# Performance work log

Hardware: AMD Instinct MI355X
Metric: run time of the kernel (lower is better)

## Reference

```python
import jax, jax.numpy as jnp
import numpy as np

N = 50000
E = 300000
HOPS = 3
LAYERS = 2
HEADS = 8
D_IN = 256
D_HID = 256
D_OUT = 256
D_HEAD = D_HID // HEADS
DECAY = [float(np.exp(-0.5 * k)) for k in range(HOPS)]  # hop_decay alpha = 0.5
LRELU_ACT = 0.01   # nn.LeakyReLU default slope (activation)
LRELU_ATT = 0.2    # GATConv attention leaky_relu slope
LN_EPS = 1e-5


def setup_inputs() -> dict:
    key = jax.random.key(0)
    ks = jax.random.split(key, 12)
    def sc(fan):
        return 1.0 / np.sqrt(fan)
    inp = {
        "x": jax.random.normal(ks[0], (N, D_IN), jnp.float32),
        "edge_index_k_hops": jax.random.randint(ks[1], (HOPS, 2, E), 0, N, jnp.int32),
        "lin1_w": jax.random.normal(ks[2], (D_IN, D_HID), jnp.float32) * sc(D_IN),
        "lin1_b": jnp.zeros((D_HID,), jnp.float32),
        "gat_w": jax.random.normal(ks[3], (LAYERS, HOPS, D_HID, D_HID), jnp.float32) * sc(D_HID),
        "gat_att_src": jax.random.normal(ks[4], (LAYERS, HOPS, HEADS, D_HEAD), jnp.float32) * sc(D_HEAD),
        "gat_att_dst": jax.random.normal(ks[5], (LAYERS, HOPS, HEADS, D_HEAD), jnp.float32) * sc(D_HEAD),
        "gat_bias": jnp.zeros((LAYERS, HOPS, D_HID), jnp.float32),
        "dec_w": jax.random.normal(ks[6], (LAYERS, HOPS, D_HID, D_OUT), jnp.float32) * sc(D_HID),
        "dec_b": jnp.zeros((LAYERS, HOPS, D_OUT), jnp.float32),
        "ln_scale": jnp.ones((LAYERS, D_OUT), jnp.float32),
        "ln_bias": jnp.zeros((LAYERS, D_OUT), jnp.float32),
    }
    return inp


def gat_conv(x, src, dst, W, a_src, a_dst, bias):
    # x: [N, D_HID]; src/dst: [E] ints. PyG GATConv (concat=True), eval mode.
    h = (x @ W).reshape(N, HEADS, D_HEAD)                  # [N, H, Dh]
    alpha_s = jnp.einsum('nhd,hd->nh', h, a_src)           # [N, H]
    alpha_d = jnp.einsum('nhd,hd->nh', h, a_dst)           # [N, H]
    e = jax.nn.leaky_relu(alpha_s[src] + alpha_d[dst], LRELU_ATT)  # [E, H]
    m = jax.ops.segment_max(e, dst, num_segments=N)        # segment softmax over dst
    e = jnp.exp(e - m[dst])
    s = jax.ops.segment_sum(e, dst, num_segments=N)
    a = e / (s[dst] + 1e-16)                               # [E, H]
    msg = h[src] * a[:, :, None]                           # [E, H, Dh]
    out = jax.ops.segment_sum(msg, dst, num_segments=N)    # [N, H, Dh]
    return out.reshape(N, D_HID) + bias


def layer_norm(x, scale, bias):
    mu = jnp.mean(x, axis=-1, keepdims=True)
    var = jnp.mean(jnp.square(x - mu), axis=-1, keepdims=True)
    return (x - mu) * jax.lax.rsqrt(var + LN_EPS) * scale + bias


def reference(x, edge_index_k_hops, lin1_w, lin1_b, gat_w, gat_att_src, gat_att_dst,
              gat_bias, dec_w, dec_b, ln_scale, ln_bias):
    h = jax.nn.leaky_relu(x @ lin1_w + lin1_b, LRELU_ACT)
    residual = h
    for l in range(LAYERS):
        acc = jnp.zeros((N, D_OUT), h.dtype)
        for k in range(HOPS):
            src = edge_index_k_hops[k, 0]
            dst = edge_index_k_hops[k, 1]
            xk = gat_conv(h, src, dst, gat_w[l, k], gat_att_src[l, k],
                          gat_att_dst[l, k], gat_bias[l, k])
            xk = jax.nn.leaky_relu(xk @ dec_w[l, k] + dec_b[l, k], LRELU_ACT)
            acc = acc + DECAY[k] * xk
        h = layer_norm(acc, ln_scale[l], ln_bias[l]) + residual
        residual = h
    return h
```

## Files before the change

### kernel.cpp

```cpp
#include <hip/hip_runtime.h>
#include <hip/hip_bf16.h>

#define NNODE 50000
#define NEDGE 300000
#define KPAD 40

static const float DECAY0 = 1.0f;
static const float DECAY1 = 0.60653065971263342f;
static const float DECAY2 = 0.36787944117144233f;

typedef __attribute__((ext_vector_type(8))) short bf16x8;
typedef __attribute__((ext_vector_type(4))) float f32x4;
typedef __attribute__((ext_vector_type(4))) unsigned short u16x4;

__device__ __forceinline__ unsigned split2(float f) {
    const unsigned u = __float_as_uint(f);
    const unsigned hi = u >> 16;
    const float fh = __uint_as_float(hi << 16);
    const unsigned lo = __float_as_uint(f - fh) >> 16;
    return (hi << 16) | lo;
}
__device__ __forceinline__ float bf2f(unsigned short u) {
    return __uint_as_float((unsigned)u << 16);
}

__global__ __launch_bounds__(256) void transpose_split_w(
    const float* __restrict__ gat_w, const float* __restrict__ dec_w,
    const float* __restrict__ lin1_w, unsigned short* __restrict__ Wp)
{
    const int m = blockIdx.z;
    const float* src = (m < 6) ? gat_w + (size_t)m * 65536
                     : (m < 12) ? dec_w + (size_t)(m - 6) * 65536
                                : lin1_w;
    unsigned short* dst = Wp + (size_t)m * 131072;
    __shared__ float tile[32][33];
    const int bx = blockIdx.x * 32;
    const int by = blockIdx.y * 32;
    const int tx = threadIdx.x & 31;
    const int ty = threadIdx.x >> 5;
#pragma unroll
    for (int i = 0; i < 32; i += 8)
        tile[ty + i][tx] = src[(size_t)(by + ty + i) * 256 + bx + tx];
    __syncthreads();
#pragma unroll
    for (int i = 0; i < 32; i += 8) {
        const int n = bx + ty + i, k = by + tx;
        const unsigned p = split2(tile[tx][ty + i]);
        dst[(size_t)n * 512 + k] = (unsigned short)(p >> 16);
        dst[(size_t)n * 512 + 256 + k] = (unsigned short)(p & 0xffffu);
    }
}

__global__ __launch_bounds__(256) void convert_split(
    const float* __restrict__ src, unsigned short* __restrict__ dst)
{
    const int gid = blockIdx.x * 256 + threadIdx.x;
    if (gid >= NNODE * 32) return;
    const int row = gid >> 5;
    const int k = (gid & 31) * 8;
    const float4 f0 = *reinterpret_cast<const float4*>(src + (size_t)row * 256 + k);
    const float4 f1 = *reinterpret_cast<const float4*>(src + (size_t)row * 256 + k + 4);
    u16x4 h0, h1, l0, l1;
    unsigned p;
    p = split2(f0.x); h0[0] = (unsigned short)(p >> 16); l0[0] = (unsigned short)p;
    p = split2(f0.y); h0[1] = (unsigned short)(p >> 16); l0[1] = (unsigned short)p;
    p = split2(f0.z); h0[2] = (unsigned short)(p >> 16); l0[2] = (unsigned short)p;
    p = split2(f0.w); h0[3] = (unsigned short)(p >> 16); l0[3] = (unsigned short)p;
    p = split2(f1.x); h1[0] = (unsigned short)(p >> 16); l1[0] = (unsigned short)p;
    p = split2(f1.y); h1[1] = (unsigned short)(p >> 16); l1[1] = (unsigned short)p;
    p = split2(f1.z); h1[2] = (unsigned short)(p >> 16); l1[2] = (unsigned short)p;
    p = split2(f1.w); h1[3] = (unsigned short)(p >> 16); l1[3] = (unsigned short)p;
    unsigned short* dh = dst + (size_t)row * 512 + k;
    *(u16x4*)dh = h0; *(u16x4*)(dh + 4) = h1;
    *(u16x4*)(dh + 256) = l0; *(u16x4*)(dh + 260) = l1;
}

__global__ __launch_bounds__(256) void gemm_pack(
    const unsigned short* __restrict__ Ap, const unsigned short* __restrict__ Wp,
    float* __restrict__ C, unsigned short* __restrict__ Cpack,
    int M, const float* __restrict__ out_bias,
    float slope, int do_act, int accum, float decay)
{
    __shared__ unsigned short Ah[128][KPAD];
    __shared__ unsigned short Al[128][KPAD];
    __shared__ unsigned short Bh[128][KPAD];
    __shared__ unsigned short Bl[128][KPAD];

    const int tid  = threadIdx.x;
    const int bm   = blockIdx.x * 128;
    const int bn   = blockIdx.y * 128;
    const int lane = tid & 63;
    const int w    = tid >> 6;
    const int wm   = w >> 1, wn = w & 1;
    const int srow = tid >> 1;
    const int skb  = (tid & 1) << 4;

    const bool aval = (bm + srow) < M;
    const unsigned short* ap = Ap + (size_t)(bm + srow) * 512 + skb;
    const unsigned short* bp = Wp + (size_t)(bn + srow) * 512 + skb;

    bf16x8 rAh0 = {0,0,0,0,0,0,0,0}, rAh1 = rAh0, rAl0 = rAh0, rAl1 = rAh0;
    bf16x8 rBh0, rBh1, rBl0, rBl1;

#define LOADT(K0)                                                        \
    do {                                                                 \
        if (aval) {                                                      \
            rAh0 = *(const bf16x8*)(ap + (K0));                          \
            rAh1 = *(const bf16x8*)(ap + (K0) + 8);                      \
            rAl0 = *(const bf16x8*)(ap + 256 + (K0));                    \
            rAl1 = *(const bf16x8*)(ap + 256 + (K0) + 8);                \
        }                                                                \
        rBh0 = *(const bf16x8*)(bp + (K0));                              \
        rBh1 = *(const bf16x8*)(bp + (K0) + 8);                          \
        rBl0 = *(const bf16x8*)(bp + 256 + (K0));                        \
        rBl1 = *(const bf16x8*)(bp + 256 + (K0) + 8);                    \
    } while (0)

    f32x4 acc[4][4];
#pragma unroll
    for (int mi = 0; mi < 4; mi++)
#pragma unroll
        for (int ni = 0; ni < 4; ni++) {
            acc[mi][ni][0] = 0.f; acc[mi][ni][1] = 0.f;
            acc[mi][ni][2] = 0.f; acc[mi][ni][3] = 0.f;
        }

    const int lrow = lane & 15;
    const int koff = (lane >> 4) << 3;

    LOADT(0);

    for (int kt = 0; kt < 8; kt++) {
        __syncthreads();
        *(bf16x8*)&Ah[srow][skb]     = rAh0;
        *(bf16x8*)&Ah[srow][skb + 8] = rAh1;
        *(bf16x8*)&Al[srow][skb]     = rAl0;
        *(bf16x8*)&Al[srow][skb + 8] = rAl1;
        *(bf16x8*)&Bh[srow][skb]     = rBh0;
        *(bf16x8*)&Bh[srow][skb + 8] = rBh1;
        *(bf16x8*)&Bl[srow][skb]     = rBl0;
        *(bf16x8*)&Bl[srow][skb + 8] = rBl1;
        __syncthreads();
        if (kt < 7) LOADT((kt + 1) * 32);

        bf16x8 fah[4], fal[4];
#pragma unroll
        for (int mi = 0; mi < 4; mi++) {
            const int r = 64 * wm + 16 * mi + lrow;
            fah[mi] = *(const bf16x8*)&Ah[r][koff];
            fal[mi] = *(const bf16x8*)&Al[r][koff];
        }
#pragma unroll
        for (int ni = 0; ni < 4; ni++) {
            const int r = 64 * wn + 16 * ni + lrow;
            const bf16x8 fbh = *(const bf16x8*)&Bh[r][koff];
            const bf16x8 fbl = *(const bf16x8*)&Bl[r][koff];
#pragma unroll
            for (int mi = 0; mi < 4; mi++) {
                acc[mi][ni] = __builtin_amdgcn_mfma_f32_16x16x32_bf16(fah[mi], fbh, acc[mi][ni], 0, 0, 0);
                acc[mi][ni] = __builtin_amdgcn_mfma_f32_16x16x32_bf16(fal[mi], fbh, acc[mi][ni], 0, 0, 0);
                acc[mi][ni] = __builtin_amdgcn_mfma_f32_16x16x32_bf16(fah[mi], fbl, acc[mi][ni], 0, 0, 0);
            }
        }
    }
#undef LOADT

    const int rb = bm + 64 * wm + ((lane >> 4) << 2);
    const int cb = bn + 64 * wn + (lane & 15);
#pragma unroll
    for (int ni = 0; ni < 4; ni++) {
        const int col = cb + 16 * ni;
        const float ob = out_bias ? out_bias[col] : 0.f;
#pragma unroll
        for (int mi = 0; mi < 4; mi++) {
#pragma unroll
            for (int r = 0; r < 4; r++) {
                const int row = rb + 16 * mi + r;
                if (row < M) {
                    float vv = acc[mi][ni][r] + ob;
                    if (do_act) vv = (vv > 0.f) ? vv : slope * vv;
                    vv *= decay;
                    if (Cpack) {
                        const unsigned p = split2(vv);
                        Cpack[(size_t)row * 512 + col] = (unsigned short)(p >> 16);
                        Cpack[(size_t)row * 512 + 256 + col] = (unsigned short)(p & 0xffffu);
                    } else if (accum) {
                        C[(size_t)row * 256 + col] += vv;
                    } else {
                        C[(size_t)row * 256 + col] = vv;
                    }
                }
            }
        }
    }
}

__global__ __launch_bounds__(256) void alpha_kernel(
    const float* __restrict__ hproj, const float* __restrict__ att_s,
    const float* __restrict__ att_d, float* __restrict__ alpha_s, float* __restrict__ alpha_d)
{
    const int n = blockIdx.x;
    const int t = threadIdx.x;
    const float v  = hproj[(size_t)n * 256 + t];
    float ps = v * att_s[t];
    float pd = v * att_d[t];
#pragma unroll
    for (int off = 16; off > 0; off >>= 1) {
        ps += __shfl_xor(ps, off, 32);
        pd += __shfl_xor(pd, off, 32);
    }
    if ((t & 31) == 0) {
        alpha_s[n * 8 + (t >> 5)] = ps;
        alpha_d[n * 8 + (t >> 5)] = pd;
    }
}

__global__ __launch_bounds__(256) void hist_kernel(
    const int* __restrict__ edges, int* __restrict__ hist)
{
    const int gid = blockIdx.x * 256 + threadIdx.x;
    if (gid >= 3 * NEDGE) return;
    const int k = gid / NEDGE;
    const int e = gid - k * NEDGE;
    const int d = edges[(size_t)k * 2 * NEDGE + NEDGE + e];
    atomicAdd(&hist[k * NNODE + d], 1);
}

__global__ __launch_bounds__(1024) void scan_kernel(
    const int* __restrict__ hist, int* __restrict__ row_ptr)
{
    const int hop = blockIdx.x;
    const int* hsrc = hist + hop * NNODE;
    int* rp = row_ptr + hop * (NNODE + 1);
    __shared__ int buf[1024];
    const int t = threadIdx.x;
    int offset = 0;
    for (int base = 0; base < NNODE; base += 1024) {
        const int idx = base + t;
        int v = (idx < NNODE) ? hsrc[idx] : 0;
        buf[t] = v;
        __syncthreads();
        for (int off = 1; off < 1024; off <<= 1) {
            int add = (t >= off) ? buf[t - off] : 0;
            __syncthreads();
            buf[t] += add;
            __syncthreads();
        }
        if (idx < NNODE) rp[idx] = offset + buf[t] - v;
        const int total = buf[1023];
        __syncthreads();
        offset += total;
    }
    if (t == 0) rp[NNODE] = offset;
}

__global__ __launch_bounds__(256) void cursor_kernel(
    const int* __restrict__ row_ptr, int* __restrict__ cursor)
{
    const int gid = blockIdx.x * 256 + threadIdx.x;
    if (gid >= 3 * NNODE) return;
    const int k = gid / NNODE;
    const int i = gid - k * NNODE;
    cursor[gid] = row_ptr[k * (NNODE + 1) + i];
}

__global__ __launch_bounds__(256) void fill_kernel(
    const int* __restrict__ edges, int* __restrict__ cursor, int* __restrict__ col)
{
    const int gid = blockIdx.x * 256 + threadIdx.x;
    if (gid >= 3 * NEDGE) return;
    const int k = gid / NEDGE;
    const int e = gid - k * NEDGE;
    const int s = edges[(size_t)k * 2 * NEDGE + e];
    const int d = edges[(size_t)k * 2 * NEDGE + NEDGE + e];
    const int pos = atomicAdd(&cursor[k * NNODE + d], 1);
    col[(size_t)k * NEDGE + pos] = s;
}

__global__ __launch_bounds__(256) void gat_gather(
    const int* __restrict__ row_ptr, const int* __restrict__ col,
    const float* __restrict__ alpha_s, const float* __restrict__ alpha_d,
    const float* __restrict__ hproj, const float* __restrict__ bias,
    unsigned short* __restrict__ outp)
{
    const int wave = (blockIdx.x * 256 + threadIdx.x) >> 6;
    const int lane = threadIdx.x & 63;
    if (wave >= NNODE) return;
    const int d = wave;
    const int h = lane >> 3;
    const float adh = alpha_d[d * 8 + h];
    const int beg = row_ptr[d];
    const int end = row_ptr[d + 1];

    float m = -3.402823466e38f;
    float s = 0.f;
    float a0 = 0.f, a1 = 0.f, a2 = 0.f, a3 = 0.f;

    for (int e = beg; e < end; ++e) {
        const int sidx = col[e];
        float v = alpha_s[sidx * 8 + h] + adh;
        v = (v > 0.f) ? v : 0.2f * v;
        if (v > m) {
            const float f = __expf(m - v);
            s *= f; a0 *= f; a1 *= f; a2 *= f; a3 *= f;
            m = v;
        }
        const float p = __expf(v - m);
        s += p;
        const float4 hv = *reinterpret_cast<const float4*>(hproj + (size_t)sidx * 256 + lane * 4);
        a0 += p * hv.x; a1 += p * hv.y; a2 += p * hv.z; a3 += p * hv.w;
    }
    const float inv = 1.f / (s + 1e-16f);
    const float b0 = bias[lane * 4 + 0], b1 = bias[lane * 4 + 1];
    const float b2 = bias[lane * 4 + 2], b3 = bias[lane * 4 + 3];
    u16x4 hi, lo;
    unsigned p0 = split2(a0 * inv + b0);
    unsigned p1 = split2(a1 * inv + b1);
    unsigned p2 = split2(a2 * inv + b2);
    unsigned p3 = split2(a3 * inv + b3);
    hi[0] = (unsigned short)(p0 >> 16); lo[0] = (unsigned short)p0;
    hi[1] = (unsigned short)(p1 >> 16); lo[1] = (unsigned short)p1;
    hi[2] = (unsigned short)(p2 >> 16); lo[2] = (unsigned short)p2;
    hi[3] = (unsigned short)(p3 >> 16); lo[3] = (unsigned short)p3;
    *(u16x4*)(outp + (size_t)d * 512 + lane * 4) = hi;
    *(u16x4*)(outp + (size_t)d * 512 + 256 + lane * 4) = lo;
}

__global__ __launch_bounds__(256) void ln_kernel(
    const float* __restrict__ accb, const unsigned short* __restrict__ hres,
    unsigned short* __restrict__ hout, float* __restrict__ final_out,
    const float* __restrict__ lns, const float* __restrict__ lnb)
{
    const int n = blockIdx.x;
    const int t = threadIdx.x;
    const float a = accb[(size_t)n * 256 + t];
    __shared__ float red[256];
    red[t] = a;
    __syncthreads();
    for (int off = 128; off > 0; off >>= 1) {
        if (t < off) red[t] += red[t + off];
        __syncthreads();
    }
    const float mu = red[0] * (1.f / 256.f);
    __syncthreads();
    const float dv = a - mu;
    red[t] = dv * dv;
    __syncthreads();
    for (int off = 128; off > 0; off >>= 1) {
        if (t < off) red[t] += red[t + off];
        __syncthreads();
    }
    const float var = red[0] * (1.f / 256.f);
    const float r = rsqrtf(var + 1e-5f);
    const float res = bf2f(hres[(size_t)n * 512 + t]) + bf2f(hres[(size_t)n * 512 + 256 + t]);
    const float o = dv * r * lns[t] + lnb[t] + res;
    if (final_out) {
        final_out[(size_t)n * 256 + t] = o;
    } else {
        const unsigned p = split2(o);
        hout[(size_t)n * 512 + t] = (unsigned short)(p >> 16);
        hout[(size_t)n * 512 + 256 + t] = (unsigned short)(p & 0xffffu);
    }
}

extern "C" void kernel_launch(void* const* d_in, const int* in_sizes, int n_in,
                              void* d_out, int out_size, void* d_ws, size_t ws_size,
                              hipStream_t stream) {
    const float* x      = (const float*)d_in[0];
    const int*   edges  = (const int*)  d_in[1];
    const float* lin1_w = (const float*)d_in[2];
    const float* lin1_b = (const float*)d_in[3];
    const float* gat_w  = (const float*)d_in[4];
    const float* att_s  = (const float*)d_in[5];
    const float* att_d  = (const float*)d_in[6];
    const float* gat_b  = (const float*)d_in[7];
    const float* dec_w  = (const float*)d_in[8];
    const float* dec_b  = (const float*)d_in[9];
    const float* ln_s   = (const float*)d_in[10];
    const float* ln_b   = (const float*)d_in[11];

    float* out = (float*)d_out;
    const size_t NF = (size_t)NNODE * 256;
    const size_t NP = (size_t)NNODE * 512;
    const size_t N8 = (size_t)NNODE * 8;

    float*          acc_buf = (float*)d_ws;
    float*          hproj   = acc_buf + NF;
    unsigned short* gpack   = (unsigned short*)(hproj + NF);
    unsigned short* hpack   = gpack + NP;
    unsigned short* wpack   = hpack + NP;
    float*          as_     = (float*)(wpack + (size_t)13 * 131072);
    float*          ad_     = as_ + N8;
    int*            hist    = (int*)(ad_ + N8);
    int*            cursor  = hist + 3 * NNODE;
    int*            row_ptr = cursor + 3 * NNODE;
    int*            col     = row_ptr + 3 * (NNODE + 1);

    const float decays[3] = {DECAY0, DECAY1, DECAY2};

    dim3 gg((NNODE + 127) / 128, 2);
    dim3 tg(8, 8, 13);
    const int e3b = (3 * NEDGE + 255) / 256;
    const int n3b = (3 * NNODE + 255) / 256;
    const int gb  = (NNODE * 64 + 255) / 256;
    const int cvb = (NNODE * 32 + 255) / 256;

    transpose_split_w<<<tg, 256, 0, stream>>>(gat_w, dec_w, lin1_w, wpack);
    convert_split<<<cvb, 256, 0, stream>>>(x, gpack);

    (void)hipMemsetAsync(hist, 0, 3 * NNODE * sizeof(int), stream);
    hist_kernel<<<e3b, 256, 0, stream>>>(edges, hist);
    scan_kernel<<<3, 1024, 0, stream>>>(hist, row_ptr);
    cursor_kernel<<<n3b, 256, 0, stream>>>(row_ptr, cursor);
    fill_kernel<<<e3b, 256, 0, stream>>>(edges, cursor, col);

    gemm_pack<<<gg, 256, 0, stream>>>(gpack, wpack + (size_t)12 * 131072, nullptr, hpack,
                                      NNODE, lin1_b, 0.01f, 1, 0, 1.f);

    for (int l = 0; l < 2; l++) {
        for (int k = 0; k < 3; k++) {
            const int lk = l * 3 + k;
            gemm_pack<<<gg, 256, 0, stream>>>(hpack, wpack + (size_t)lk * 131072, hproj, nullptr,
                                              NNODE, nullptr, 0.f, 0, 0, 1.f);
            alpha_kernel<<<NNODE, 256, 0, stream>>>(hproj, att_s + lk * 256, att_d + lk * 256,
                                                    as_, ad_);
            gat_gather<<<gb, 256, 0, stream>>>(row_ptr + (size_t)k * (NNODE + 1),
                                               col + (size_t)k * NEDGE,
                                               as_, ad_, hproj, gat_b + lk * 256, gpack);
            gemm_pack<<<gg, 256, 0, stream>>>(gpack, wpack + (size_t)(6 + lk) * 131072, acc_buf,
                                              nullptr, NNODE, dec_b + lk * 256,
                                              0.01f, 1, (k > 0) ? 1 : 0, decays[k]);
        }
        ln_kernel<<<NNODE, 256, 0, stream>>>(acc_buf, hpack, hpack,
                                             (l == 1) ? out : nullptr,
                                             ln_s + l * 256, ln_b + l * 256);
    }
}
```

Baseline: 1.686 ms.

## Store projected features as bf16 payload and parallelize CSR prefix scan

The GAT projection GEMM now writes round-to-nearest bf16 values instead of fp32, and the alpha and gather kernels read them. This halves the bytes moved in the edge-gather phase, which reads a random source row for every edge. The single-block sequential scan is replaced by a three-kernel block-local scan, block-sum scan and add that also fills the cursor array. The trade-off is lower precision in the aggregated features (bf16 instead of fp32) and a few extra kernel launches.

```diff
diff --git a/kernel.cpp b/kernel.cpp
--- a/kernel.cpp
+++ b/kernel.cpp
@@ -22,6 +22,10 @@
 }
 __device__ __forceinline__ float bf2f(unsigned short u) {
     return __uint_as_float((unsigned)u << 16);
+}
+__device__ __forceinline__ unsigned short rn_bf16(float f) {
+    const unsigned u = __float_as_uint(f);
+    return (unsigned short)((u + 0x7fffu + ((u >> 16) & 1u)) >> 16);
 }
 
 __global__ __launch_bounds__(256) void transpose_split_w(
@@ -78,6 +82,7 @@
 __global__ __launch_bounds__(256) void gemm_pack(
     const unsigned short* __restrict__ Ap, const unsigned short* __restrict__ Wp,
     float* __restrict__ C, unsigned short* __restrict__ Cpack,
+    unsigned short* __restrict__ payload,
     int M, const float* __restrict__ out_bias,
     float slope, int do_act, int accum, float decay)
 {
@@ -177,17 +182,21 @@
             for (int r = 0; r < 4; r++) {
                 const int row = rb + 16 * mi + r;
                 if (row < M) {
-                    float vv = acc[mi][ni][r] + ob;
-                    if (do_act) vv = (vv > 0.f) ? vv : slope * vv;
-                    vv *= decay;
-                    if (Cpack) {
-                        const unsigned p = split2(vv);
-                        Cpack[(size_t)row * 512 + col] = (unsigned short)(p >> 16);
-                        Cpack[(size_t)row * 512 + 256 + col] = (unsigned short)(p & 0xffffu);
-                    } else if (accum) {
-                        C[(size_t)row * 256 + col] += vv;
+                    if (payload) {
+                        payload[(size_t)row * 256 + col] = rn_bf16(acc[mi][ni][r]);
                     } else {
-                        C[(size_t)row * 256 + col] = vv;
+                        float vv = acc[mi][ni][r] + ob;
+                        if (do_act) vv = (vv > 0.f) ? vv : slope * vv;
+                        vv *= decay;
+                        if (Cpack) {
+                            const unsigned p = split2(vv);
+                            Cpack[(size_t)row * 512 + col] = (unsigned short)(p >> 16);
+                            Cpack[(size_t)row * 512 + 256 + col] = (unsigned short)(p & 0xffffu);
+                        } else if (accum) {
+                            C[(size_t)row * 256 + col] += vv;
+                        } else {
+                            C[(size_t)row * 256 + col] = vv;
+                        }
                     }
                 }
             }
@@ -196,12 +205,12 @@
 }
 
 __global__ __launch_bounds__(256) void alpha_kernel(
-    const float* __restrict__ hproj, const float* __restrict__ att_s,
+    const unsigned short* __restrict__ payload, const float* __restrict__ att_s,
     const float* __restrict__ att_d, float* __restrict__ alpha_s, float* __restrict__ alpha_d)
 {
     const int n = blockIdx.x;
     const int t = threadIdx.x;
-    const float v  = hproj[(size_t)n * 256 + t];
+    const float v  = bf2f(payload[(size_t)n * 256 + t]);
     float ps = v * att_s[t];
     float pd = v * att_d[t];
 #pragma unroll
@@ -226,42 +235,64 @@
     atomicAdd(&hist[k * NNODE + d], 1);
 }
 
-__global__ __launch_bounds__(1024) void scan_kernel(
-    const int* __restrict__ hist, int* __restrict__ row_ptr)
+__global__ __launch_bounds__(256) void scan_local(
+    const int* __restrict__ hist, int* __restrict__ loc, int* __restrict__ bsums)
+{
+    const int hop = blockIdx.y;
+    const int base = blockIdx.x * 1024;
+    const int t = threadIdx.x;
+    const int idx = base + t * 4;
+    int4 v = make_int4(0, 0, 0, 0);
+    if (idx < NNODE)
+        v = *reinterpret_cast<const int4*>(hist + (size_t)hop * NNODE + idx);
+    const int s = v.x + v.y + v.z + v.w;
+    __shared__ int buf[256];
+    buf[t] = s;
+    __syncthreads();
+    for (int off = 1; off < 256; off <<= 1) {
+        const int a = (t >= off) ? buf[t - off] : 0;
+        __syncthreads();
+        buf[t] += a;
+        __syncthreads();
+    }
+    const int excl = buf[t] - s;
+    if (t == 255) bsums[hop * 64 + blockIdx.x] = buf[255];
+    if (idx < NNODE) {
+        int* lp = loc + (size_t)hop * NNODE + idx;
+        lp[0] = excl;
+        lp[1] = excl + v.x;
+        lp[2] = excl + v.x + v.y;
+        lp[3] = excl + v.x + v.y + v.z;
+    }
+}
+
+__global__ __launch_bounds__(64) void scan_bsums(
+    int* __restrict__ bsums, int* __restrict__ row_ptr)
 {
     const int hop = blockIdx.x;
-    const int* hsrc = hist + hop * NNODE;
-    int* rp = row_ptr + hop * (NNODE + 1);
-    __shared__ int buf[1024];
-    const int t = threadIdx.x;
-    int offset = 0;
-    for (int base = 0; base < NNODE; base += 1024) {
-        const int idx = base + t;
-        int v = (idx < NNODE) ? hsrc[idx] : 0;
-        buf[t] = v;
-        __syncthreads();
-        for (int off = 1; off < 1024; off <<= 1) {
-            int add = (t >= off) ? buf[t - off] : 0;
-            __syncthreads();
-            buf[t] += add;
-            __syncthreads();
-        }
-        if (idx < NNODE) rp[idx] = offset + buf[t] - v;
-        const int total = buf[1023];
-        __syncthreads();
-        offset += total;
-    }
-    if (t == 0) rp[NNODE] = offset;
-}
-
-__global__ __launch_bounds__(256) void cursor_kernel(
-    const int* __restrict__ row_ptr, int* __restrict__ cursor)
+    const int lane = threadIdx.x;
+    const int v = (lane < 49) ? bsums[hop * 64 + lane] : 0;
+    int incl = v;
+#pragma unroll
+    for (int m = 1; m < 64; m <<= 1) {
+        const int o = __shfl_up(incl, m, 64);
+        if (lane >= m) incl += o;
+    }
+    if (lane < 49) bsums[hop * 64 + lane] = incl - v;
+    if (lane == 48) row_ptr[hop * (NNODE + 1) + NNODE] = incl;
+}
+
+__global__ __launch_bounds__(256) void scan_add(
+    const int* __restrict__ loc, const int* __restrict__ bsums,
+    int* __restrict__ row_ptr, int* __restrict__ cursor)
 {
     const int gid = blockIdx.x * 256 + threadIdx.x;
     if (gid >= 3 * NNODE) return;
     const int k = gid / NNODE;
     const int i = gid - k * NNODE;
-    cursor[gid] = row_ptr[k * (NNODE + 1) + i];
+    const int v = loc[gid] + bsums[k * 64 + (i >> 10)];
+    row_ptr[k * (NNODE + 1) + i] = v;
+    cursor[gid] = v;
 }
 
 __global__ __launch_bounds__(256) void fill_kernel(
@@ -280,7 +311,7 @@
 __global__ __launch_bounds__(256) void gat_gather(
     const int* __restrict__ row_ptr, const int* __restrict__ col,
     const float* __restrict__ alpha_s, const float* __restrict__ alpha_d,
-    const float* __restrict__ hproj, const float* __restrict__ bias,
+    const unsigned short* __restrict__ payload, const float* __restrict__ bias,
     unsigned short* __restrict__ outp)
 {
     const int wave = (blockIdx.x * 256 + threadIdx.x) >> 6;
@@ -307,8 +338,9 @@
         }
         const float p = __expf(v - m);
         s += p;
-        const float4 hv = *reinterpret_cast<const float4*>(hproj + (size_t)sidx * 256 + lane * 4);
-        a0 += p * hv.x; a1 += p * hv.y; a2 += p * hv.z; a3 += p * hv.w;
+        const u16x4 hv = *reinterpret_cast<const u16x4*>(payload + (size_t)sidx * 256 + lane * 4);
+        a0 += p * bf2f(hv[0]); a1 += p * bf2f(hv[1]);
+        a2 += p * bf2f(hv[2]); a3 += p * bf2f(hv[3]);
     }
     const float inv = 1.f / (s + 1e-16f);
     const float b0 = bias[lane * 4 + 0], b1 = bias[lane * 4 + 1];
@@ -385,8 +417,8 @@
     const size_t N8 = (size_t)NNODE * 8;
 
     float*          acc_buf = (float*)d_ws;
-    float*          hproj   = acc_buf + NF;
-    unsigned short* gpack   = (unsigned short*)(hproj + NF);
+    unsigned short* payload = (unsigned short*)(acc_buf + NF);
+    unsigned short* gpack   = payload + NF;
     unsigned short* hpack   = gpack + NP;
     unsigned short* wpack   = hpack + NP;
     float*          as_     = (float*)(wpack + (size_t)13 * 131072);
@@ -395,11 +427,14 @@
     int*            cursor  = hist + 3 * NNODE;
     int*            row_ptr = cursor + 3 * NNODE;
     int*            col     = row_ptr + 3 * (NNODE + 1);
+    int*            loc     = col + 3 * NEDGE;
+    int*            bsums   = loc + 3 * NNODE;
 
     const float decays[3] = {DECAY0, DECAY1, DECAY2};
 
     dim3 gg((NNODE + 127) / 128, 2);
     dim3 tg(8, 8, 13);
+    dim3 sg(49, 3);
     const int e3b = (3 * NEDGE + 255) / 256;
     const int n3b = (3 * NNODE + 255) / 256;
     const int gb  = (NNODE * 64 + 255) / 256;
@@ -410,25 +445,28 @@
 
     (void)hipMemsetAsync(hist, 0, 3 * NNODE * sizeof(int), stream);
     hist_kernel<<<e3b, 256, 0, stream>>>(edges, hist);
-    scan_kernel<<<3, 1024, 0, stream>>>(hist, row_ptr);
-    cursor_kernel<<<n3b, 256, 0, stream>>>(row_ptr, cursor);
+    scan_local<<<sg, 256, 0, stream>>>(hist, loc, bsums);
+    scan_bsums<<<3, 64, 0, stream>>>(bsums, row_ptr);
+    scan_add<<<n3b, 256, 0, stream>>>(loc, bsums, row_ptr, cursor);
     fill_kernel<<<e3b, 256, 0, stream>>>(edges, cursor, col);
 
-    gemm_pack<<<gg, 256, 0, stream>>>(gpack, wpack + (size_t)12 * 131072, nullptr, hpack,
+    gemm_pack<<<gg, 256, 0, stream>>>(gpack, wpack + (size_t)12 * 131072, nullptr, hpack, nullptr,
                                       NNODE, lin1_b, 0.01f, 1, 0, 1.f);
 
     for (int l = 0; l < 2; l++) {
         for (int k = 0; k < 3; k++) {
             const int lk = l * 3 + k;
-            gemm_pack<<<gg, 256, 0, stream>>>(hpack, wpack + (size_t)lk * 131072, hproj, nullptr,
+            gemm_pack<<<gg, 256, 0, stream>>>(hpack, wpack + (size_t)lk * 131072,
+                                              nullptr, nullptr, payload,
                                               NNODE, nullptr, 0.f, 0, 0, 1.f);
-            alpha_kernel<<<NNODE, 256, 0, stream>>>(hproj, att_s + lk * 256, att_d + lk * 256,
+            alpha_kernel<<<NNODE, 256, 0, stream>>>(payload, att_s + lk * 256, att_d + lk * 256,
                                                     as_, ad_);
             gat_gather<<<gb, 256, 0, stream>>>(row_ptr + (size_t)k * (NNODE + 1),
                                                col + (size_t)k * NEDGE,
-                                               as_, ad_, hproj, gat_b + lk * 256, gpack);
-            gemm_pack<<<gg, 256, 0, stream>>>(gpack, wpack + (size_t)(6 + lk) * 131072, acc_buf,
-                                              nullptr, NNODE, dec_b + lk * 256,
+                                               as_, ad_, payload, gat_b + lk * 256, gpack);
+            gemm_pack<<<gg, 256, 0, stream>>>(gpack, wpack + (size_t)(6 + lk) * 131072,
+                                              acc_buf, nullptr, nullptr,
+                                              NNODE, dec_b + lk * 256,
                                               0.01f, 1, (k > 0) ? 1 : 0, decays[k]);
         }
         ln_kernel<<<NNODE, 256, 0, stream>>>(acc_buf, hpack, hpack,
```

Result: faster. 1.501 ms (-11.0%).
